# Optimization experiments

Measured on AMD Instinct MI355X. Metric: run time of the kernel, lower is better.

## Reference

```python
import jax, jax.numpy as jnp
import numpy as np

WINDOW = 128  # causal window width
D_SCALE = None  # set from val dim at trace time


def _softsign(x):
    return x / (1.0 + jnp.abs(x))


def setup_inputs() -> dict:
    key = jax.random.key(0)
    k1, k2 = jax.random.split(key)
    B, N, D = 4, 4096, 256
    val = jax.random.normal(k1, (B, N, D), dtype=jnp.float32)
    state = jax.random.normal(k2, (B, N), dtype=jnp.float32)
    return {"val": val, "state": state}


def reference(val, state):
    # val: [B, N, D], state: [B, N]
    B, N, D = val.shape
    # pairwise_fn: scaled dot product -> scores [B, N, N]
    scores = jnp.einsum('bnd,bmd->bnm', val, val) / jnp.sqrt(jnp.asarray(D, val.dtype))
    # edge_compress_fn: softsign
    edges = _softsign(scores)
    # causal window mask: source j satisfies (j <= i) & (j >= i - window)
    i = jnp.arange(N)[:, None]
    j = jnp.arange(N)[None, :]
    mask = (j <= i) & (j >= i - WINDOW)  # [N, N]
    edges = edges * mask[None, :, :].astype(edges.dtype)
    # val_proj_fn / state_proj_fn are Identity
    delta_state = jnp.einsum('bij,bj->bi', edges, state)   # [B, N]
    delta_val = jnp.einsum('bij,bjd->bid', edges, val)      # [B, N, D]
    return (delta_state, delta_val)
```

## Files before the change

kernel.cpp:

```cpp
#include <hip/hip_runtime.h>

#define NSEQ 4096
#define DIM  256
#define WIN  128
#define BATCH 4

typedef __bf16 bf16x8 __attribute__((ext_vector_type(8)));
typedef float  f32x4  __attribute__((ext_vector_type(4)));
typedef int    v2i    __attribute__((ext_vector_type(2)));
typedef int    v4i    __attribute__((ext_vector_type(4)));

__device__ __forceinline__ int sub_off(int j, int d) {
    return (((j >> 2) * 16 + (d >> 4)) << 6) + ((j & 3) << 4) + (d & 15);
}

__device__ __forceinline__ unsigned short f2bf(float f) {
    unsigned u = __builtin_bit_cast(unsigned, f);
    u += 0x7fffu + ((u >> 16) & 1u);
    return (unsigned short)(u >> 16);
}

__device__ __forceinline__ unsigned pk2bf(float lo, float hi) {
    unsigned r;
    asm("v_cvt_pk_bf16_f32 %0, %1, %2" : "=v"(r) : "v"(lo), "v"(hi));
    return r;
}

__global__ __launch_bounds__(256, 3)
void sp_kernel(const float* __restrict__ val,
               const float* __restrict__ state,
               float* __restrict__ out) {
    __shared__ __align__(128) unsigned short vbuf[2][8192];
    __shared__ __align__(128) unsigned short E_s[32 * 56];
    __shared__ float ds_part[4][16];

    const int bx  = blockIdx.x;
    const int lbx = ((bx & 7) << 6) + (bx >> 3);
    const int b      = lbx >> 7;
    const int tile_i = lbx & 127;
    const int r0     = tile_i << 5;

    const int t   = threadIdx.x;
    const int w   = t >> 6;
    const int l   = t & 63;
    const int l15 = l & 15;
    const int l4  = l >> 4;
    const int mt  = w >> 1;
    const int jt  = w & 1;

    const float* valb = val + ((size_t)b * NSEQ) * DIM;
    const float* stb  = state + ((size_t)b * NSEQ);
    float* out_state  = out + ((size_t)b * NSEQ);
    float* out_val    = out + (size_t)BATCH * NSEQ + ((size_t)b * NSEQ) * DIM;

    const int s_jl0 = (w << 2) + l4;
    const int s_jl1 = s_jl0 + 16;

    {
        const float* src = valb + ((size_t)tile_i << 13);
        #pragma unroll
        for (int qq = 0; qq < 8; ++qq) {
            const int jl2 = (qq & 1) ? s_jl1 : s_jl0;
            const int d0 = (l15 << 2) + ((qq >> 1) << 6);
            float4 v = *reinterpret_cast<const float4*>(src + jl2 * DIM + d0);
            uint2 u;
            u.x = pk2bf(v.x, v.y);
            u.y = pk2bf(v.z, v.w);
            *reinterpret_cast<uint2*>(&vbuf[0][sub_off(jl2, d0)]) = u;
        }
    }
    __syncthreads();

    const int il = (mt << 4) + l15;
    const int jl = (jt << 4) + l15;
    bf16x8 af[8];
    #pragma unroll
    for (int ks = 0; ks < 8; ++ks)
        af[ks] = *reinterpret_cast<const bf16x8*>(&vbuf[0][sub_off(il, (l4 << 3) + (ks << 5))]);

    const int tj0   = (tile_i >= 4) ? (tile_i - 4) : 0;
    const int ntile = tile_i - tj0 + 1;

    float dsacc[4] = {0.f, 0.f, 0.f, 0.f};
    f32x4 accpv[2][4];
    #pragma unroll
    for (int m2 = 0; m2 < 2; ++m2)
        #pragma unroll
        for (int tt = 0; tt < 4; ++tt)
            accpv[m2][tt] = (f32x4){0.f, 0.f, 0.f, 0.f};

    int p = 0;
    for (int q = 0; q < ntile; ++q) {
        const int ti = tile_i - q;
        const bool havenext = (q + 1 < ntile);
        const unsigned short* bp = &vbuf[p][0];
        unsigned short* bn = &vbuf[1 - p][0];

        const int jg = (ti << 5) + jl;
        const float stv = stb[jg];

        bf16x8 sb[8];
        #pragma unroll
        for (int ks = 0; ks < 8; ++ks)
            sb[ks] = *reinterpret_cast<const bf16x8*>(&bp[sub_off(jl, (l4 << 3) + (ks << 5))]);
        f32x4 acc = (f32x4){0.f, 0.f, 0.f, 0.f};
        #pragma unroll
        for (int ks = 0; ks < 8; ++ks)
            acc = __builtin_amdgcn_mfma_f32_16x16x32_bf16(af[ks], sb[ks], acc, 0, 0, 0);

        const int ib = r0 + (mt << 4) + (l4 << 2);
        #pragma unroll
        for (int r = 0; r < 4; ++r) {
            float s = acc[r] * 0.0625f;
            float e = s * __builtin_amdgcn_rcpf(1.0f + fabsf(s));
            const int ig = ib + r;
            if (jg > ig || jg < ig - WIN) e = 0.0f;
            dsacc[r] += e * stv;
            E_s[((mt << 4) + (l4 << 2) + r) * 56 + (jt << 4) + l15] = f2bf(e);
        }

        if (havenext) {
            const float* src = valb + ((size_t)(ti - 1) << 13);
            #pragma unroll
            for (int qq = 0; qq < 8; ++qq) {
                const int jl2 = (qq & 1) ? s_jl1 : s_jl0;
                const int d0  = (l15 << 2) + ((qq >> 1) << 6);
                float4 v = *reinterpret_cast<const float4*>(src + jl2 * DIM + d0);
                uint2 u;
                u.x = pk2bf(v.x, v.y);
                u.y = pk2bf(v.z, v.w);
                *reinterpret_cast<uint2*>(&bn[sub_off(jl2, d0)]) = u;
            }
        }
        __syncthreads();

        bf16x8 ef0 = *reinterpret_cast<const bf16x8*>(&E_s[l15 * 56 + (l4 << 3)]);
        bf16x8 ef1 = *reinterpret_cast<const bf16x8*>(&E_s[(16 + l15) * 56 + (l4 << 3)]);
        const unsigned lds_base = (unsigned)(size_t)bp;
        v2i tr[8];
        #pragma unroll
        for (int tt = 0; tt < 4; ++tt) {
            const int nt = (w << 2) + tt;
            unsigned a0 = lds_base + (unsigned)((((l4 << 5) + nt) << 7) + (l15 << 3));
            asm volatile("ds_read_b64_tr_b16 %0, %1" : "=v"(tr[2 * tt]) : "v"(a0));
            asm volatile("ds_read_b64_tr_b16 %0, %1 offset:2048" : "=v"(tr[2 * tt + 1]) : "v"(a0));
        }
        asm volatile("s_waitcnt lgkmcnt(0)" ::: "memory");
        __builtin_amdgcn_sched_barrier(0);
        #pragma unroll
        for (int tt = 0; tt < 4; ++tt) {
            v4i tmp;
            tmp.x = tr[2 * tt].x;     tmp.y = tr[2 * tt].y;
            tmp.z = tr[2 * tt + 1].x; tmp.w = tr[2 * tt + 1].y;
            bf16x8 bfr = __builtin_bit_cast(bf16x8, tmp);
            accpv[0][tt] = __builtin_amdgcn_mfma_f32_16x16x32_bf16(ef0, bfr, accpv[0][tt], 0, 0, 0);
            accpv[1][tt] = __builtin_amdgcn_mfma_f32_16x16x32_bf16(ef1, bfr, accpv[1][tt], 0, 0, 0);
        }
        if (havenext) __syncthreads();
        p ^= 1;
    }

    #pragma unroll
    for (int m = 1; m <= 8; m <<= 1) {
        #pragma unroll
        for (int r = 0; r < 4; ++r)
            dsacc[r] += __shfl_xor(dsacc[r], m, 64);
    }
    if (l15 == 0) {
        #pragma unroll
        for (int r = 0; r < 4; ++r)
            ds_part[w][(l4 << 2) + r] = dsacc[r];
    }
    __syncthreads();
    if (t < 32) {
        const int m2 = t >> 4;
        out_state[r0 + t] = ds_part[(m2 << 1)][t & 15] + ds_part[(m2 << 1) + 1][t & 15];
    }

    #pragma unroll
    for (int m2 = 0; m2 < 2; ++m2) {
        #pragma unroll
        for (int tt = 0; tt < 4; ++tt) {
            const int d = (w << 6) + (tt << 4) + l15;
            #pragma unroll
            for (int r = 0; r < 4; ++r) {
                const int ig = r0 + (m2 << 4) + (l4 << 2) + r;
                out_val[(size_t)ig * DIM + d] = accpv[m2][tt][r];
            }
        }
    }
}

extern "C" void kernel_launch(void* const* d_in, const int* in_sizes, int n_in,
                              void* d_out, int out_size, void* d_ws, size_t ws_size,
                              hipStream_t stream) {
    const float* val   = (const float*)d_in[0];
    const float* state = (const float*)d_in[1];
    float* out = (float*)d_out;
    sp_kernel<<<dim3(BATCH * (NSEQ / 32)), dim3(256), 0, stream>>>(val, state, out);
}
```

Baseline: 16.40 us.

## Split key tiles across waves and reduce partial outputs through LDS

```diff
diff --git a/kernel.cpp b/kernel.cpp
--- a/kernel.cpp
+++ b/kernel.cpp
@@ -4,6 +4,7 @@
 #define DIM  256
 #define WIN  128
 #define BATCH 4
+#define ESTR 56
 
 typedef __bf16 bf16x8 __attribute__((ext_vector_type(8)));
 typedef float  f32x4  __attribute__((ext_vector_type(4)));
@@ -26,13 +27,13 @@
     return r;
 }
 
-__global__ __launch_bounds__(256, 3)
+__global__ __launch_bounds__(256, 2)
 void sp_kernel(const float* __restrict__ val,
                const float* __restrict__ state,
                float* __restrict__ out) {
-    __shared__ __align__(128) unsigned short vbuf[2][8192];
-    __shared__ __align__(128) unsigned short E_s[32 * 56];
-    __shared__ float ds_part[4][16];
+    __shared__ __align__(128) unsigned short V[4][8192];
+    __shared__ __align__(128) unsigned short Ebuf[4][32 * ESTR];
+    __shared__ float ds_part[4][32];
 
     const int bx  = blockIdx.x;
     const int lbx = ((bx & 7) << 6) + (bx >> 3);
@@ -45,149 +46,178 @@
     const int l   = t & 63;
     const int l15 = l & 15;
     const int l4  = l >> 4;
-    const int mt  = w >> 1;
-    const int jt  = w & 1;
 
     const float* valb = val + ((size_t)b * NSEQ) * DIM;
     const float* stb  = state + ((size_t)b * NSEQ);
     float* out_state  = out + ((size_t)b * NSEQ);
     float* out_val    = out + (size_t)BATCH * NSEQ + ((size_t)b * NSEQ) * DIM;
 
-    const int s_jl0 = (w << 2) + l4;
-    const int s_jl1 = s_jl0 + 16;
-
-    {
-        const float* src = valb + ((size_t)tile_i << 13);
-        #pragma unroll
-        for (int qq = 0; qq < 8; ++qq) {
-            const int jl2 = (qq & 1) ? s_jl1 : s_jl0;
-            const int d0 = (l15 << 2) + ((qq >> 1) << 6);
-            float4 v = *reinterpret_cast<const float4*>(src + jl2 * DIM + d0);
-            uint2 u;
-            u.x = pk2bf(v.x, v.y);
-            u.y = pk2bf(v.z, v.w);
-            *reinterpret_cast<uint2*>(&vbuf[0][sub_off(jl2, d0)]) = u;
-        }
-    }
-    __syncthreads();
-
-    const int il = (mt << 4) + l15;
-    const int jl = (jt << 4) + l15;
-    bf16x8 af[8];
-    #pragma unroll
-    for (int ks = 0; ks < 8; ++ks)
-        af[ks] = *reinterpret_cast<const bf16x8*>(&vbuf[0][sub_off(il, (l4 << 3) + (ks << 5))]);
-
     const int tj0   = (tile_i >= 4) ? (tile_i - 4) : 0;
     const int ntile = tile_i - tj0 + 1;
 
-    float dsacc[4] = {0.f, 0.f, 0.f, 0.f};
-    f32x4 accpv[2][4];
+    bf16x8 af2[2][8];
+    #pragma unroll
+    for (int m2 = 0; m2 < 2; ++m2) {
+        const float* rp = valb + (size_t)(r0 + (m2 << 4) + l15) * DIM + (l4 << 3);
+        #pragma unroll
+        for (int ks = 0; ks < 8; ++ks) {
+            float4 u0 = *reinterpret_cast<const float4*>(rp + (ks << 5));
+            float4 u1 = *reinterpret_cast<const float4*>(rp + (ks << 5) + 4);
+            v4i pw;
+            pw.x = pk2bf(u0.x, u0.y);
+            pw.y = pk2bf(u0.z, u0.w);
+            pw.z = pk2bf(u1.x, u1.y);
+            pw.w = pk2bf(u1.z, u1.w);
+            af2[m2][ks] = __builtin_bit_cast(bf16x8, pw);
+        }
+    }
+
+    unsigned short* Vw = &V[w][0];
+    unsigned short* Ew = &Ebuf[w][0];
+
+    float dsacc[2][4];
     #pragma unroll
     for (int m2 = 0; m2 < 2; ++m2)
         #pragma unroll
-        for (int tt = 0; tt < 4; ++tt)
-            accpv[m2][tt] = (f32x4){0.f, 0.f, 0.f, 0.f};
-
-    int p = 0;
-    for (int q = 0; q < ntile; ++q) {
-        const int ti = tile_i - q;
-        const bool havenext = (q + 1 < ntile);
-        const unsigned short* bp = &vbuf[p][0];
-        unsigned short* bn = &vbuf[1 - p][0];
-
-        const int jg = (ti << 5) + jl;
-        const float stv = stb[jg];
-
-        bf16x8 sb[8];
-        #pragma unroll
-        for (int ks = 0; ks < 8; ++ks)
-            sb[ks] = *reinterpret_cast<const bf16x8*>(&bp[sub_off(jl, (l4 << 3) + (ks << 5))]);
-        f32x4 acc = (f32x4){0.f, 0.f, 0.f, 0.f};
-        #pragma unroll
-        for (int ks = 0; ks < 8; ++ks)
-            acc = __builtin_amdgcn_mfma_f32_16x16x32_bf16(af[ks], sb[ks], acc, 0, 0, 0);
-
-        const int ib = r0 + (mt << 4) + (l4 << 2);
-        #pragma unroll
-        for (int r = 0; r < 4; ++r) {
-            float s = acc[r] * 0.0625f;
-            float e = s * __builtin_amdgcn_rcpf(1.0f + fabsf(s));
-            const int ig = ib + r;
-            if (jg > ig || jg < ig - WIN) e = 0.0f;
-            dsacc[r] += e * stv;
-            E_s[((mt << 4) + (l4 << 2) + r) * 56 + (jt << 4) + l15] = f2bf(e);
+        for (int r = 0; r < 4; ++r)
+            dsacc[m2][r] = 0.f;
+
+    f32x4 accpv[2][16];
+    #pragma unroll
+    for (int m2 = 0; m2 < 2; ++m2)
+        #pragma unroll
+        for (int nt = 0; nt < 16; ++nt)
+            accpv[m2][nt] = (f32x4){0.f, 0.f, 0.f, 0.f};
+
+    #pragma unroll
+    for (int pass = 0; pass < 2; ++pass) {
+        const int tq = w + (pass << 2);
+        if (tq < ntile) {
+            const int ti = tj0 + tq;
+            const int jb = ti << 5;
+
+            {
+                const float* src = valb + ((size_t)ti << 13);
+                #pragma unroll
+                for (int qq = 0; qq < 32; ++qq) {
+                    const int jl = ((qq & 7) << 2) + l4;
+                    const int d0 = (l15 << 2) + ((qq >> 3) << 6);
+                    float4 v = *reinterpret_cast<const float4*>(src + jl * DIM + d0);
+                    uint2 u;
+                    u.x = pk2bf(v.x, v.y);
+                    u.y = pk2bf(v.z, v.w);
+                    *reinterpret_cast<uint2*>(&Vw[sub_off(jl, d0)]) = u;
+                }
+            }
+
+            f32x4 qacc[2][2];
+            #pragma unroll
+            for (int jt2 = 0; jt2 < 2; ++jt2) {
+                bf16x8 sb[8];
+                #pragma unroll
+                for (int ks = 0; ks < 8; ++ks)
+                    sb[ks] = *reinterpret_cast<const bf16x8*>(&Vw[sub_off((jt2 << 4) + l15, (l4 << 3) + (ks << 5))]);
+                #pragma unroll
+                for (int m2 = 0; m2 < 2; ++m2) {
+                    qacc[m2][jt2] = (f32x4){0.f, 0.f, 0.f, 0.f};
+                    #pragma unroll
+                    for (int ks = 0; ks < 8; ++ks)
+                        qacc[m2][jt2] = __builtin_amdgcn_mfma_f32_16x16x32_bf16(af2[m2][ks], sb[ks], qacc[m2][jt2], 0, 0, 0);
+                }
+            }
+
+            #pragma unroll
+            for (int m2 = 0; m2 < 2; ++m2)
+                #pragma unroll
+                for (int jt2 = 0; jt2 < 2; ++jt2) {
+                    const int jg = jb + (jt2 << 4) + l15;
+                    const float stv = stb[jg];
+                    #pragma unroll
+                    for (int r = 0; r < 4; ++r) {
+                        const int ig = r0 + (m2 << 4) + (l4 << 2) + r;
+                        float s = qacc[m2][jt2][r] * 0.0625f;
+                        float e = s * __builtin_amdgcn_rcpf(1.0f + fabsf(s));
+                        if (jg > ig || jg < ig - WIN) e = 0.0f;
+                        dsacc[m2][r] += e * stv;
+                        Ew[((m2 << 4) + (l4 << 2) + r) * ESTR + (jt2 << 4) + l15] = f2bf(e);
+                    }
+                }
+
+            bf16x8 ef0 = *reinterpret_cast<const bf16x8*>(&Ew[l15 * ESTR + (l4 << 3)]);
+            bf16x8 ef1 = *reinterpret_cast<const bf16x8*>(&Ew[(16 + l15) * ESTR + (l4 << 3)]);
+            const unsigned lds_base = (unsigned)(size_t)Vw;
+            #pragma unroll
+            for (int g = 0; g < 4; ++g) {
+                v2i tr[8];
+                #pragma unroll
+                for (int h = 0; h < 4; ++h) {
+                    const int nt = (g << 2) + h;
+                    unsigned a0 = lds_base + (unsigned)((((l4 << 5) + nt) << 7) + (l15 << 3));
+                    asm volatile("ds_read_b64_tr_b16 %0, %1" : "=v"(tr[2 * h]) : "v"(a0));
+                    asm volatile("ds_read_b64_tr_b16 %0, %1 offset:2048" : "=v"(tr[2 * h + 1]) : "v"(a0));
+                }
+                asm volatile("s_waitcnt lgkmcnt(0)" ::: "memory");
+                __builtin_amdgcn_sched_barrier(0);
+                #pragma unroll
+                for (int h = 0; h < 4; ++h) {
+                    const int nt = (g << 2) + h;
+                    v4i tmp;
+                    tmp.x = tr[2 * h].x;     tmp.y = tr[2 * h].y;
+                    tmp.z = tr[2 * h + 1].x; tmp.w = tr[2 * h + 1].y;
+                    bf16x8 bfr = __builtin_bit_cast(bf16x8, tmp);
+                    accpv[0][nt] = __builtin_amdgcn_mfma_f32_16x16x32_bf16(ef0, bfr, accpv[0][nt], 0, 0, 0);
+                    accpv[1][nt] = __builtin_amdgcn_mfma_f32_16x16x32_bf16(ef1, bfr, accpv[1][nt], 0, 0, 0);
+                }
+            }
         }
-
-        if (havenext) {
-            const float* src = valb + ((size_t)(ti - 1) << 13);
-            #pragma unroll
-            for (int qq = 0; qq < 8; ++qq) {
-                const int jl2 = (qq & 1) ? s_jl1 : s_jl0;
-                const int d0  = (l15 << 2) + ((qq >> 1) << 6);
-                float4 v = *reinterpret_cast<const float4*>(src + jl2 * DIM + d0);
-                uint2 u;
-                u.x = pk2bf(v.x, v.y);
-                u.y = pk2bf(v.z, v.w);
-                *reinterpret_cast<uint2*>(&bn[sub_off(jl2, d0)]) = u;
-            }
+    }
+
+    #pragma unroll
+    for (int m = 1; m <= 8; m <<= 1)
+        #pragma unroll
+        for (int m2 = 0; m2 < 2; ++m2)
+            #pragma unroll
+            for (int r = 0; r < 4; ++r)
+                dsacc[m2][r] += __shfl_xor(dsacc[m2][r], m, 64);
+    if (l15 == 0) {
+        #pragma unroll
+        for (int m2 = 0; m2 < 2; ++m2)
+            #pragma unroll
+            for (int r = 0; r < 4; ++r)
+                ds_part[w][(m2 << 4) + (l4 << 2) + r] = dsacc[m2][r];
+    }
+    __syncthreads();
+    if (t < 32)
+        out_state[r0 + t] = ds_part[0][t] + ds_part[1][t] + ds_part[2][t] + ds_part[3][t];
+
+    float* red = reinterpret_cast<float*>(&V[0][0]);
+    #pragma unroll
+    for (int c = 0; c < 4; ++c) {
+        __syncthreads();
+        #pragma unroll
+        for (int m2 = 0; m2 < 2; ++m2)
+            #pragma unroll
+            for (int h = 0; h < 4; ++h) {
+                const int nt = (c << 2) + h;
+                const int row = (m2 << 4) + (l4 << 2);
+                const int col = (h << 4) + l15;
+                #pragma unroll
+                for (int r = 0; r < 4; ++r)
+                    red[(w << 11) + (row + r) * 64 + col] = accpv[m2][nt][r];
+            }
+        __syncthreads();
+        const int row = t >> 3;
+        const int colb = (t & 7) << 3;
+        f32x4 s0 = *reinterpret_cast<const f32x4*>(&red[row * 64 + colb]);
+        f32x4 s1 = *reinterpret_cast<const f32x4*>(&red[row * 64 + colb + 4]);
+        #pragma unroll
+        for (int ww = 1; ww < 4; ++ww) {
+            s0 += *reinterpret_cast<const f32x4*>(&red[(ww << 11) + row * 64 + colb]);
+            s1 += *reinterpret_cast<const f32x4*>(&red[(ww << 11) + row * 64 + colb + 4]);
         }
-        __syncthreads();
-
-        bf16x8 ef0 = *reinterpret_cast<const bf16x8*>(&E_s[l15 * 56 + (l4 << 3)]);
-        bf16x8 ef1 = *reinterpret_cast<const bf16x8*>(&E_s[(16 + l15) * 56 + (l4 << 3)]);
-        const unsigned lds_base = (unsigned)(size_t)bp;
-        v2i tr[8];
-        #pragma unroll
-        for (int tt = 0; tt < 4; ++tt) {
-            const int nt = (w << 2) + tt;
-            unsigned a0 = lds_base + (unsigned)((((l4 << 5) + nt) << 7) + (l15 << 3));
-            asm volatile("ds_read_b64_tr_b16 %0, %1" : "=v"(tr[2 * tt]) : "v"(a0));
-            asm volatile("ds_read_b64_tr_b16 %0, %1 offset:2048" : "=v"(tr[2 * tt + 1]) : "v"(a0));
-        }
-        asm volatile("s_waitcnt lgkmcnt(0)" ::: "memory");
-        __builtin_amdgcn_sched_barrier(0);
-        #pragma unroll
-        for (int tt = 0; tt < 4; ++tt) {
-            v4i tmp;
-            tmp.x = tr[2 * tt].x;     tmp.y = tr[2 * tt].y;
-            tmp.z = tr[2 * tt + 1].x; tmp.w = tr[2 * tt + 1].y;
-            bf16x8 bfr = __builtin_bit_cast(bf16x8, tmp);
-            accpv[0][tt] = __builtin_amdgcn_mfma_f32_16x16x32_bf16(ef0, bfr, accpv[0][tt], 0, 0, 0);
-            accpv[1][tt] = __builtin_amdgcn_mfma_f32_16x16x32_bf16(ef1, bfr, accpv[1][tt], 0, 0, 0);
-        }
-        if (havenext) __syncthreads();
-        p ^= 1;
-    }
-
-    #pragma unroll
-    for (int m = 1; m <= 8; m <<= 1) {
-        #pragma unroll
-        for (int r = 0; r < 4; ++r)
-            dsacc[r] += __shfl_xor(dsacc[r], m, 64);
-    }
-    if (l15 == 0) {
-        #pragma unroll
-        for (int r = 0; r < 4; ++r)
-            ds_part[w][(l4 << 2) + r] = dsacc[r];
-    }
-    __syncthreads();
-    if (t < 32) {
-        const int m2 = t >> 4;
-        out_state[r0 + t] = ds_part[(m2 << 1)][t & 15] + ds_part[(m2 << 1) + 1][t & 15];
-    }
-
-    #pragma unroll
-    for (int m2 = 0; m2 < 2; ++m2) {
-        #pragma unroll
-        for (int tt = 0; tt < 4; ++tt) {
-            const int d = (w << 6) + (tt << 4) + l15;
-            #pragma unroll
-            for (int r = 0; r < 4; ++r) {
-                const int ig = r0 + (m2 << 4) + (l4 << 2) + r;
-                out_val[(size_t)ig * DIM + d] = accpv[m2][tt][r];
-            }
-        }
+        float* dst = out_val + (size_t)(r0 + row) * DIM + (c << 6) + colb;
+        *reinterpret_cast<f32x4*>(dst)     = s0;
+        *reinterpret_cast<f32x4*>(dst + 4) = s1;
     }
 }
 
```

After: 28.66 us. +74.7%, slower.

## Halve query tile to 16 rows, doubling block count, iterate key tiles forward

Applied to the files above, without the earlier changes.

```diff
diff --git a/kernel.cpp b/kernel.cpp
--- a/kernel.cpp
+++ b/kernel.cpp
@@ -4,6 +4,7 @@
 #define DIM  256
 #define WIN  128
 #define BATCH 4
+#define ESTR 40
 
 typedef __bf16 bf16x8 __attribute__((ext_vector_type(8)));
 typedef float  f32x4  __attribute__((ext_vector_type(4)));
@@ -31,21 +32,20 @@
                const float* __restrict__ state,
                float* __restrict__ out) {
     __shared__ __align__(128) unsigned short vbuf[2][8192];
-    __shared__ __align__(128) unsigned short E_s[32 * 56];
-    __shared__ float ds_part[4][16];
+    __shared__ __align__(128) unsigned short E_s[16 * ESTR];
+    __shared__ float ds_part[2][16];
 
     const int bx  = blockIdx.x;
-    const int lbx = ((bx & 7) << 6) + (bx >> 3);
-    const int b      = lbx >> 7;
-    const int tile_i = lbx & 127;
-    const int r0     = tile_i << 5;
+    const int lbx = ((bx & 7) << 7) + (bx >> 3);
+    const int b      = lbx >> 8;
+    const int tile16 = lbx & 255;
+    const int i0     = tile16 << 4;
 
     const int t   = threadIdx.x;
     const int w   = t >> 6;
     const int l   = t & 63;
     const int l15 = l & 15;
     const int l4  = l >> 4;
-    const int mt  = w >> 1;
     const int jt  = w & 1;
 
     const float* valb = val + ((size_t)b * NSEQ) * DIM;
@@ -56,8 +56,28 @@
     const int s_jl0 = (w << 2) + l4;
     const int s_jl1 = s_jl0 + 16;
 
+    const int tj0   = (i0 >= WIN) ? ((i0 - WIN) >> 5) : 0;
+    const int lastt = i0 >> 5;
+    const int ntile = lastt - tj0 + 1;
+
+    bf16x8 af[8];
     {
-        const float* src = valb + ((size_t)tile_i << 13);
+        const float* rp = valb + (size_t)(i0 + l15) * DIM + (l4 << 3);
+        #pragma unroll
+        for (int ks = 0; ks < 8; ++ks) {
+            float4 u0 = *reinterpret_cast<const float4*>(rp + (ks << 5));
+            float4 u1 = *reinterpret_cast<const float4*>(rp + (ks << 5) + 4);
+            v4i pw;
+            pw.x = pk2bf(u0.x, u0.y);
+            pw.y = pk2bf(u0.z, u0.w);
+            pw.z = pk2bf(u1.x, u1.y);
+            pw.w = pk2bf(u1.z, u1.w);
+            af[ks] = __builtin_bit_cast(bf16x8, pw);
+        }
+    }
+
+    {
+        const float* src = valb + ((size_t)tj0 << 13);
         #pragma unroll
         for (int qq = 0; qq < 8; ++qq) {
             const int jl2 = (qq & 1) ? s_jl1 : s_jl0;
@@ -71,56 +91,47 @@
     }
     __syncthreads();
 
-    const int il = (mt << 4) + l15;
-    const int jl = (jt << 4) + l15;
-    bf16x8 af[8];
+    float dsacc[4] = {0.f, 0.f, 0.f, 0.f};
+    f32x4 accpv[4];
     #pragma unroll
-    for (int ks = 0; ks < 8; ++ks)
-        af[ks] = *reinterpret_cast<const bf16x8*>(&vbuf[0][sub_off(il, (l4 << 3) + (ks << 5))]);
-
-    const int tj0   = (tile_i >= 4) ? (tile_i - 4) : 0;
-    const int ntile = tile_i - tj0 + 1;
-
-    float dsacc[4] = {0.f, 0.f, 0.f, 0.f};
-    f32x4 accpv[2][4];
-    #pragma unroll
-    for (int m2 = 0; m2 < 2; ++m2)
-        #pragma unroll
-        for (int tt = 0; tt < 4; ++tt)
-            accpv[m2][tt] = (f32x4){0.f, 0.f, 0.f, 0.f};
+    for (int tt = 0; tt < 4; ++tt)
+        accpv[tt] = (f32x4){0.f, 0.f, 0.f, 0.f};
 
     int p = 0;
     for (int q = 0; q < ntile; ++q) {
-        const int ti = tile_i - q;
+        const int ti = tj0 + q;
         const bool havenext = (q + 1 < ntile);
         const unsigned short* bp = &vbuf[p][0];
         unsigned short* bn = &vbuf[1 - p][0];
-
-        const int jg = (ti << 5) + jl;
-        const float stv = stb[jg];
-
-        bf16x8 sb[8];
-        #pragma unroll
-        for (int ks = 0; ks < 8; ++ks)
-            sb[ks] = *reinterpret_cast<const bf16x8*>(&bp[sub_off(jl, (l4 << 3) + (ks << 5))]);
-        f32x4 acc = (f32x4){0.f, 0.f, 0.f, 0.f};
-        #pragma unroll
-        for (int ks = 0; ks < 8; ++ks)
-            acc = __builtin_amdgcn_mfma_f32_16x16x32_bf16(af[ks], sb[ks], acc, 0, 0, 0);
-
-        const int ib = r0 + (mt << 4) + (l4 << 2);
-        #pragma unroll
-        for (int r = 0; r < 4; ++r) {
-            float s = acc[r] * 0.0625f;
-            float e = s * __builtin_amdgcn_rcpf(1.0f + fabsf(s));
-            const int ig = ib + r;
-            if (jg > ig || jg < ig - WIN) e = 0.0f;
-            dsacc[r] += e * stv;
-            E_s[((mt << 4) + (l4 << 2) + r) * 56 + (jt << 4) + l15] = f2bf(e);
+        const int jb = ti << 5;
+
+        if (w < 2) {
+            const int jl = (jt << 4) + l15;
+            const int jg = jb + jl;
+            const float stv = stb[jg];
+
+            bf16x8 sb[8];
+            #pragma unroll
+            for (int ks = 0; ks < 8; ++ks)
+                sb[ks] = *reinterpret_cast<const bf16x8*>(&bp[sub_off(jl, (l4 << 3) + (ks << 5))]);
+            f32x4 acc = (f32x4){0.f, 0.f, 0.f, 0.f};
+            #pragma unroll
+            for (int ks = 0; ks < 8; ++ks)
+                acc = __builtin_amdgcn_mfma_f32_16x16x32_bf16(af[ks], sb[ks], acc, 0, 0, 0);
+
+            #pragma unroll
+            for (int r = 0; r < 4; ++r) {
+                float s = acc[r] * 0.0625f;
+                float e = s * __builtin_amdgcn_rcpf(1.0f + fabsf(s));
+                const int ig = i0 + (l4 << 2) + r;
+                if (jg > ig || jg < ig - WIN) e = 0.0f;
+                dsacc[r] += e * stv;
+                E_s[((l4 << 2) + r) * ESTR + (jt << 4) + l15] = f2bf(e);
+            }
         }
 
         if (havenext) {
-            const float* src = valb + ((size_t)(ti - 1) << 13);
+            const float* src = valb + ((size_t)(ti + 1) << 13);
             #pragma unroll
             for (int qq = 0; qq < 8; ++qq) {
                 const int jl2 = (qq & 1) ? s_jl1 : s_jl0;
@@ -134,8 +145,7 @@
         }
         __syncthreads();
 
-        bf16x8 ef0 = *reinterpret_cast<const bf16x8*>(&E_s[l15 * 56 + (l4 << 3)]);
-        bf16x8 ef1 = *reinterpret_cast<const bf16x8*>(&E_s[(16 + l15) * 56 + (l4 << 3)]);
+        bf16x8 ef = *reinterpret_cast<const bf16x8*>(&E_s[l15 * ESTR + (l4 << 3)]);
         const unsigned lds_base = (unsigned)(size_t)bp;
         v2i tr[8];
         #pragma unroll
@@ -153,40 +163,36 @@
             tmp.x = tr[2 * tt].x;     tmp.y = tr[2 * tt].y;
             tmp.z = tr[2 * tt + 1].x; tmp.w = tr[2 * tt + 1].y;
             bf16x8 bfr = __builtin_bit_cast(bf16x8, tmp);
-            accpv[0][tt] = __builtin_amdgcn_mfma_f32_16x16x32_bf16(ef0, bfr, accpv[0][tt], 0, 0, 0);
-            accpv[1][tt] = __builtin_amdgcn_mfma_f32_16x16x32_bf16(ef1, bfr, accpv[1][tt], 0, 0, 0);
+            accpv[tt] = __builtin_amdgcn_mfma_f32_16x16x32_bf16(ef, bfr, accpv[tt], 0, 0, 0);
         }
         if (havenext) __syncthreads();
         p ^= 1;
     }
 
+    if (w < 2) {
+        #pragma unroll
+        for (int m = 1; m <= 8; m <<= 1) {
+            #pragma unroll
+            for (int r = 0; r < 4; ++r)
+                dsacc[r] += __shfl_xor(dsacc[r], m, 64);
+        }
+        if (l15 == 0) {
+            #pragma unroll
+            for (int r = 0; r < 4; ++r)
+                ds_part[w][(l4 << 2) + r] = dsacc[r];
+        }
+    }
+    __syncthreads();
+    if (t < 16)
+        out_state[i0 + t] = ds_part[0][t] + ds_part[1][t];
+
     #pragma unroll
-    for (int m = 1; m <= 8; m <<= 1) {
-        #pragma unroll
-        for (int r = 0; r < 4; ++r)
-            dsacc[r] += __shfl_xor(dsacc[r], m, 64);
-    }
-    if (l15 == 0) {
-        #pragma unroll
-        for (int r = 0; r < 4; ++r)
-            ds_part[w][(l4 << 2) + r] = dsacc[r];
-    }
-    __syncthreads();
-    if (t < 32) {
-        const int m2 = t >> 4;
-        out_state[r0 + t] = ds_part[(m2 << 1)][t & 15] + ds_part[(m2 << 1) + 1][t & 15];
-    }
-
-    #pragma unroll
-    for (int m2 = 0; m2 < 2; ++m2) {
-        #pragma unroll
-        for (int tt = 0; tt < 4; ++tt) {
-            const int d = (w << 6) + (tt << 4) + l15;
-            #pragma unroll
-            for (int r = 0; r < 4; ++r) {
-                const int ig = r0 + (m2 << 4) + (l4 << 2) + r;
-                out_val[(size_t)ig * DIM + d] = accpv[m2][tt][r];
-            }
+    for (int tt = 0; tt < 4; ++tt) {
+        const int d = (((w << 2) + tt) << 4) + l15;
+        #pragma unroll
+        for (int r = 0; r < 4; ++r) {
+            const int ig = i0 + (l4 << 2) + r;
+            out_val[(size_t)ig * DIM + d] = accpv[tt][r];
         }
     }
 }
@@ -197,5 +203,5 @@
     const float* val   = (const float*)d_in[0];
     const float* state = (const float*)d_in[1];
     float* out = (float*)d_out;
-    sp_kernel<<<dim3(BATCH * (NSEQ / 32)), dim3(256), 0, stream>>>(val, state, out);
-}
+    sp_kernel<<<dim3(BATCH * (NSEQ / 16)), dim3(256), 0, stream>>>(val, state, out);
+}
```

Result: slower. 25.58 us (+55.9%).
